# Kernel tuning notes

Measured on AMD Instinct MI355X. Metric: run time of the kernel, lower is better.

The kernel has to match this reference:

```python
import jax, jax.numpy as jnp
import numpy as np

B, S, E, D, OUT = 128, 128, 256, 256, 64


def setup_inputs() -> dict:
    key = jax.random.key(0)
    ks = jax.random.split(key, 10)
    w = lambda k, shp, s=0.05: (jax.random.normal(k, shp, dtype=jnp.float32) * s)
    return {
        "input_encoded": jax.random.normal(ks[0], (B, S, E), dtype=jnp.float32),
        "y_history": jax.random.normal(ks[1], (B, S, OUT), dtype=jnp.float32),
        "h0": jax.random.normal(ks[2], (B, D), dtype=jnp.float32) * 0.1,
        "c0": jax.random.normal(ks[3], (B, D), dtype=jnp.float32) * 0.1,
        "attn_W1": w(ks[4], (2 * D + E, E)),
        "attn_b1": jnp.zeros((E,), jnp.float32),
        "attn_w2": w(ks[5], (E,)),
        "attn_b2": jnp.zeros((1,), jnp.float32),
        "lstm_Wih": w(ks[6], (OUT, 4 * D)),
        "lstm_Whh": w(ks[7], (D, 4 * D)),
        "lstm_bih": jnp.zeros((4 * D,), jnp.float32),
        "lstm_bhh": jnp.zeros((4 * D,), jnp.float32),
        "fc_W": w(ks[8], (E + OUT, OUT)),
        "fc_b": jnp.zeros((OUT,), jnp.float32),
        "fc_out_W": w(ks[9], (D + E, OUT * S)),
        "fc_out_b": jnp.zeros((OUT * S,), jnp.float32),
    }


def reference(input_encoded, y_history, h0, c0, attn_W1, attn_b1, attn_w2, attn_b2,
              lstm_Wih, lstm_Whh, lstm_bih, lstm_bhh, fc_W, fc_b, fc_out_W, fc_out_b):
    # Split the attn first-layer weight according to the concat order (h, c, enc).
    Wh, Wc, We = attn_W1[:D], attn_W1[D:2 * D], attn_W1[2 * D:]
    # Encoder projection is time-invariant across decoder steps; hoist it.
    enc_proj = jnp.einsum('bse,ef->bsf', input_encoded, We)  # [B,S,E]

    def step(carry, y_t):
        h, c, _ = carry
        hc = h @ Wh + c @ Wc + attn_b1                       # [B,E]
        pre = jnp.tanh(enc_proj + hc[:, None, :])            # [B,S,E]
        scores = pre @ attn_w2 + attn_b2[0]                  # [B,S]
        alpha = jax.nn.softmax(scores, axis=1)
        context = jnp.einsum('bs,bse->be', alpha, input_encoded)  # [B,E]
        y_tilde = jnp.concatenate([context, y_t], axis=1) @ fc_W + fc_b  # [B,OUT]
        gates = y_tilde @ lstm_Wih + lstm_bih + h @ lstm_Whh + lstm_bhh  # [B,4D]
        i, f, g, o = jnp.split(gates, 4, axis=1)  # pytorch gate order i,f,g,o
        c_new = jax.nn.sigmoid(f) * c + jax.nn.sigmoid(i) * jnp.tanh(g)
        h_new = jax.nn.sigmoid(o) * jnp.tanh(c_new)
        return (h_new, c_new, context), None

    y_seq = jnp.transpose(y_history, (1, 0, 2))  # [S,B,OUT]
    (h_T, c_T, context_T), _ = jax.lax.scan(step, (h0, c0, jnp.zeros((B, E), h0.dtype)), y_seq)
    out = jnp.concatenate([h_T, context_T], axis=1) @ fc_out_W + fc_out_b  # [B,OUT*S]
    return out.reshape(-1, S, OUT)
```

## Files before the change

kernel.cpp:

```cpp
#include <hip/hip_runtime.h>

#define BB 128
#define SS 128
#define EE 256
#define DD 256
#define OO 64

#define W1_OFF   0
#define WHH_OFF  196608
#define WIH_OFF  458752
#define FCW_OFF  524288
#define WTOTAL   544768

__device__ __forceinline__ float fsig(float x) { return 1.0f / (1.0f + __expf(-x)); }
__device__ __forceinline__ float ftanh(float x) {
    float t = __expf(-2.0f * fabsf(x));
    float r = (1.0f - t) / (1.0f + t);
    return copysignf(r, x);
}
__device__ __forceinline__ int SWZ(int e) { return (e & ~31) | ((e + 4 * (e >> 5)) & 31); }
__device__ __forceinline__ float bflo(unsigned int u) { return __uint_as_float(u << 16); }
__device__ __forceinline__ float bfhi(unsigned int u) { return __uint_as_float(u & 0xffff0000u); }

__global__ __launch_bounds__(256) void conv_kernel(
    const float* __restrict__ W1, const float* __restrict__ Whh,
    const float* __restrict__ Wih, const float* __restrict__ fcW,
    unsigned short* __restrict__ out)
{
    const int idx = blockIdx.x * 256 + threadIdx.x;
    float f;
    if      (idx < WHH_OFF)  f = W1[idx];
    else if (idx < WIH_OFF)  f = Whh[idx - WHH_OFF];
    else if (idx < FCW_OFF)  f = Wih[idx - WIH_OFF];
    else if (idx < WTOTAL)   f = fcW[idx - FCW_OFF];
    else return;
    unsigned int u = __float_as_uint(f);
    u = (u + 0x7fffu + ((u >> 16) & 1u)) >> 16;
    out[idx] = (unsigned short)u;
}

__global__ __launch_bounds__(1024, 4) void scan_kernel(
    const float* __restrict__ inp,
    const float* __restrict__ yhist,
    const float* __restrict__ h0, const float* __restrict__ c0,
    const float* __restrict__ W1f,
    const float* __restrict__ b1, const float* __restrict__ w2, const float* __restrict__ b2,
    const float* __restrict__ bih, const float* __restrict__ bhh,
    const float* __restrict__ fcb,
    const unsigned short* __restrict__ wbf,
    float* __restrict__ hctxT)
{
    __shared__ float sh_inp[SS * 260];
    __shared__ float red[5 * 1024];
    __shared__ float sh_h[DD], sh_c[DD];
    __shared__ float sh_hc[EE];
    __shared__ float sh_w2[EE];
    __shared__ float sh_raw[SS];
    __shared__ float sh_ctx[EE];
    __shared__ float sh_y[OO], sh_yt[OO];
    __shared__ float sh_misc[1];

    const int b = blockIdx.x, t = threadIdx.x;
    const float* inp_b = inp + (size_t)b * SS * EE;
    const unsigned short* W1bf  = wbf + W1_OFF;
    const unsigned short* Whhbf = wbf + WHH_OFF;
    const unsigned short* Wihbf = wbf + WIH_OFF;
    const unsigned short* fcWbf = wbf + FCW_OFF;
    const float b2v = b2[0];

    const int c0_1 = (t & 63) * 4,  kg1 = t >> 6;
    const int c0_2 = (t & 255) * 4, kg2 = t >> 8;
    const int s_own = t >> 3, a2 = t & 7, e0 = a2 * 32;
    const int c0_3 = (t & 127) * 2, sg3 = t >> 7;
    const int o4 = (t & 15) * 4, kc3 = t >> 4;

    const float bs_reg  = bih[t] + bhh[t];
    const float fcb_reg = (t < 64) ? fcb[t] : 0.f;

    #pragma unroll
    for (int i = 0; i < 8; ++i) {
        const int idx = i * 1024 + t;
        const int s = idx >> 6, c4 = (idx & 63) * 4;
        *(float4*)&sh_inp[s * 260 + c4] = *(const float4*)(inp_b + (size_t)idx * 4);
    }
    if (t < 256) {
        sh_h[t] = h0[b * 256 + t]; sh_c[t] = c0[b * 256 + t];
        sh_w2[SWZ(t)] = w2[t];
    }
    __syncthreads();

    float er[32];
    #pragma unroll
    for (int j = 0; j < 32; ++j) er[j] = 0.f;
    {
        const float* We = W1f + 512 * 256;
        for (int kc = 0; kc < 16; ++kc) {
            {
                const int row = t >> 6, c4 = (t & 63) * 4;
                *(float4*)&red[row * 256 + c4] =
                    *(const float4*)(We + (size_t)(kc * 16 + row) * 256 + c4);
            }
            __syncthreads();
            for (int k = 0; k < 16; ++k) {
                const float xv = sh_inp[s_own * 260 + kc * 16 + k];
                #pragma unroll
                for (int j4 = 0; j4 < 8; ++j4) {
                    float4 w = *(const float4*)&red[k * 256 + e0 + j4 * 4];
                    er[j4*4+0] += xv * w.x; er[j4*4+1] += xv * w.y;
                    er[j4*4+2] += xv * w.z; er[j4*4+3] += xv * w.w;
                }
            }
            __syncthreads();
        }
        if (t < 256) red[t] = b1[t];
        __syncthreads();
        #pragma unroll
        for (int j4 = 0; j4 < 8; ++j4) {
            float4 v = *(const float4*)&red[e0 + j4 * 4];
            er[j4*4+0] += v.x; er[j4*4+1] += v.y; er[j4*4+2] += v.z; er[j4*4+3] += v.w;
        }
        __syncthreads();
    }

    for (int ts = 0; ts < SS; ++ts) {
        if (t < 64) sh_y[t] = yhist[(size_t)b * SS * OO + ts * OO + t];

        {
            float a0 = 0.f, a1 = 0.f, a2v = 0.f, a3 = 0.f;
            #pragma unroll 8
            for (int k = kg1 * 32; k < kg1 * 32 + 32; ++k) {
                const float xv = (k < 256) ? sh_h[k] : sh_c[k - 256];
                uint2 w = *(const uint2*)(W1bf + (size_t)k * 256 + c0_1);
                a0  += xv * bflo(w.x); a1 += xv * bfhi(w.x);
                a2v += xv * bflo(w.y); a3 += xv * bfhi(w.y);
            }
            *(float4*)&red[kg1 * 256 + c0_1] = make_float4(a0, a1, a2v, a3);
        }
        __syncthreads();
        if (t < 256) {
            float v = 0.f;
            #pragma unroll
            for (int kg = 0; kg < 16; ++kg) v += red[kg * 256 + t];
            sh_hc[SWZ(t)] = v;
        }
        __syncthreads();

        {
            float a0 = 0.f, a1 = 0.f, a2v = 0.f, a3 = 0.f;
            #pragma unroll 8
            for (int k = kg2 * 64; k < kg2 * 64 + 64; ++k) {
                const float hv = sh_h[k];
                uint2 w = *(const uint2*)(Whhbf + (size_t)k * 1024 + c0_2);
                a0  += hv * bflo(w.x); a1 += hv * bfhi(w.x);
                a2v += hv * bflo(w.y); a3 += hv * bfhi(w.y);
            }
            *(float4*)&red[kg2 * 1024 + c0_2] = make_float4(a0, a1, a2v, a3);
        }
        {
            float acc = 0.f;
            #pragma unroll
            for (int j4 = 0; j4 < 8; ++j4) {
                const int phys = e0 + ((j4 * 4 + 4 * a2) & 31);
                float4 hc4 = *(const float4*)&sh_hc[phys];
                float4 w24 = *(const float4*)&sh_w2[phys];
                acc += ftanh(er[j4*4+0] + hc4.x) * w24.x;
                acc += ftanh(er[j4*4+1] + hc4.y) * w24.y;
                acc += ftanh(er[j4*4+2] + hc4.z) * w24.z;
                acc += ftanh(er[j4*4+3] + hc4.w) * w24.w;
            }
            acc += __shfl_xor(acc, 1);
            acc += __shfl_xor(acc, 2);
            acc += __shfl_xor(acc, 4);
            if (a2 == 0) sh_raw[s_own] = __expf(acc + b2v);
        }
        __syncthreads();

        float gh_reg;
        {
            float v = bs_reg;
            #pragma unroll
            for (int kg = 0; kg < 4; ++kg) v += red[kg * 1024 + t];
            gh_reg = v;
        }
        if (t < 64) {
            float v = sh_raw[t] + sh_raw[t + 64];
            #pragma unroll
            for (int m = 32; m > 0; m >>= 1) v += __shfl_xor(v, m);
            if (t == 0) sh_misc[0] = 1.0f / v;
        }
        __syncthreads();

        uint2 wpre[16];
        #pragma unroll
        for (int i = 0; i < 16; ++i)
            wpre[i] = *(const uint2*)(Wihbf + (size_t)(kg2 * 16 + i) * 1024 + c0_2);
        {
            float ax = 0.f, ay = 0.f;
            #pragma unroll
            for (int i = 0; i < 16; ++i) {
                const int s = sg3 * 16 + i;
                const float al = sh_raw[s];
                ax += al * sh_inp[s * 260 + c0_3];
                ay += al * sh_inp[s * 260 + c0_3 + 1];
            }
            *(float2*)&red[sg3 * 256 + c0_3] = make_float2(ax, ay);
        }
        __syncthreads();
        if (t < 256) {
            float v = 0.f;
            #pragma unroll
            for (int sg = 0; sg < 8; ++sg) v += red[sg * 256 + t];
            v *= sh_misc[0];
            sh_ctx[t] = v;
            if (ts == SS - 1) hctxT[(size_t)(256 + t) * 128 + b] = v;
        }
        __syncthreads();

        {
            float a0 = 0.f, a1 = 0.f, a2v = 0.f, a3 = 0.f;
            for (int kk = kc3 * 5; kk < kc3 * 5 + 5; ++kk) {
                const float val = (kk < 256) ? sh_ctx[kk] : sh_y[kk - 256];
                uint2 w = *(const uint2*)(fcWbf + kk * 64 + o4);
                a0  += val * bflo(w.x); a1 += val * bfhi(w.x);
                a2v += val * bflo(w.y); a3 += val * bfhi(w.y);
            }
            *(float4*)&red[kc3 * 64 + o4] = make_float4(a0, a1, a2v, a3);
        }
        __syncthreads();
        if (t < 64) {
            float v = fcb_reg;
            #pragma unroll 16
            for (int kg = 0; kg < 64; ++kg) v += red[kg * 64 + t];
            sh_yt[t] = v;
        }
        __syncthreads();

        {
            float a0 = 0.f, a1 = 0.f, a2v = 0.f, a3 = 0.f;
            #pragma unroll
            for (int i = 0; i < 16; ++i) {
                const float yv = sh_yt[kg2 * 16 + i];
                const uint2 w = wpre[i];
                a0  += yv * bflo(w.x); a1 += yv * bfhi(w.x);
                a2v += yv * bflo(w.y); a3 += yv * bfhi(w.y);
            }
            *(float4*)&red[kg2 * 1024 + c0_2] = make_float4(a0, a1, a2v, a3);
        }
        __syncthreads();
        {
            float g = gh_reg;
            #pragma unroll
            for (int kg = 0; kg < 4; ++kg) g += red[kg * 1024 + t];
            red[4096 + t] = g;
        }
        __syncthreads();
        if (t < 256) {
            const float gi = red[4096 + t], gf = red[4096 + 256 + t];
            const float gg = red[4096 + 512 + t], go = red[4096 + 768 + t];
            const float cn = fsig(gf) * sh_c[t] + fsig(gi) * ftanh(gg);
            sh_c[t] = cn;
            const float hn = fsig(go) * ftanh(cn);
            sh_h[t] = hn;
            if (ts == SS - 1) hctxT[(size_t)t * 128 + b] = hn;
        }
        __syncthreads();
    }
}

__global__ __launch_bounds__(256) void out_gemm(
    const float* __restrict__ AT, const float* __restrict__ W,
    const float* __restrict__ bias, float* __restrict__ out)
{
    __shared__ float Ab[64 * 132];
    __shared__ float Bb[64 * 32];
    const int t = threadIdx.x;
    const int nt = blockIdx.x * 32;
    const int n4 = (t & 7) * 4;
    const int m4 = (t >> 3) * 4;
    float acc[4][4];
    #pragma unroll
    for (int i = 0; i < 4; ++i)
        #pragma unroll
        for (int jj = 0; jj < 4; ++jj) acc[i][jj] = 0.f;

    for (int kc = 0; kc < 8; ++kc) {
        #pragma unroll
        for (int i = 0; i < 8; ++i) {
            const int flat4 = i * 256 + t;
            const int row = flat4 >> 5, mm4 = (flat4 & 31) * 4;
            float4 v = *(const float4*)(AT + (size_t)(kc * 64 + row) * 128 + mm4);
            *(float4*)&Ab[row * 132 + mm4] = v;
        }
        #pragma unroll
        for (int i = 0; i < 2; ++i) {
            const int fl = t + i * 256;
            const int k = fl >> 3, nn4 = (fl & 7) * 4;
            *(float4*)&Bb[k * 32 + nn4] =
                *(const float4*)(W + (size_t)(kc * 64 + k) * 8192 + nt + nn4);
        }
        __syncthreads();
        for (int k = 0; k < 64; ++k) {
            const float4 bv = *(const float4*)&Bb[k * 32 + n4];
            const float4 av = *(const float4*)&Ab[k * 132 + m4];
            acc[0][0] += av.x * bv.x; acc[0][1] += av.x * bv.y; acc[0][2] += av.x * bv.z; acc[0][3] += av.x * bv.w;
            acc[1][0] += av.y * bv.x; acc[1][1] += av.y * bv.y; acc[1][2] += av.y * bv.z; acc[1][3] += av.y * bv.w;
            acc[2][0] += av.z * bv.x; acc[2][1] += av.z * bv.y; acc[2][2] += av.z * bv.z; acc[2][3] += av.z * bv.w;
            acc[3][0] += av.w * bv.x; acc[3][1] += av.w * bv.y; acc[3][2] += av.w * bv.z; acc[3][3] += av.w * bv.w;
        }
        __syncthreads();
    }
    const float4 bb = *(const float4*)(bias + nt + n4);
    #pragma unroll
    for (int i = 0; i < 4; ++i) {
        float4 r;
        r.x = acc[i][0] + bb.x; r.y = acc[i][1] + bb.y;
        r.z = acc[i][2] + bb.z; r.w = acc[i][3] + bb.w;
        *(float4*)(out + (size_t)(m4 + i) * 8192 + nt + n4) = r;
    }
}

extern "C" void kernel_launch(void* const* d_in, const int* in_sizes, int n_in,
                              void* d_out, int out_size, void* d_ws, size_t ws_size,
                              hipStream_t stream) {
    const float* inp = (const float*)d_in[0];
    const float* yh  = (const float*)d_in[1];
    const float* h0  = (const float*)d_in[2];
    const float* c0  = (const float*)d_in[3];
    const float* W1  = (const float*)d_in[4];
    const float* b1  = (const float*)d_in[5];
    const float* w2  = (const float*)d_in[6];
    const float* b2  = (const float*)d_in[7];
    const float* Wih = (const float*)d_in[8];
    const float* Whh = (const float*)d_in[9];
    const float* bih = (const float*)d_in[10];
    const float* bhh = (const float*)d_in[11];
    const float* fcW = (const float*)d_in[12];
    const float* fcb = (const float*)d_in[13];
    const float* foW = (const float*)d_in[14];
    const float* fob = (const float*)d_in[15];

    float* hctxT = (float*)d_ws;
    unsigned short* wbf = (unsigned short*)d_out;

    conv_kernel<<<dim3((WTOTAL + 255) / 256), dim3(256), 0, stream>>>(W1, Whh, Wih, fcW, wbf);
    scan_kernel<<<dim3(BB), dim3(1024), 0, stream>>>(
        inp, yh, h0, c0, W1, b1, w2, b2, bih, bhh, fcb, wbf, hctxT);
    out_gemm<<<dim3(8192 / 32), dim3(256), 0, stream>>>(hctxT, foW, fob, (float*)d_out);
}
```

Measured before the change: 5.672 ms.

## Restructure per-step matvecs with wider loads, shuffle reductions, register-resident weights

```diff
diff --git a/kernel.cpp b/kernel.cpp
--- a/kernel.cpp
+++ b/kernel.cpp
@@ -21,6 +21,13 @@
 __device__ __forceinline__ int SWZ(int e) { return (e & ~31) | ((e + 4 * (e >> 5)) & 31); }
 __device__ __forceinline__ float bflo(unsigned int u) { return __uint_as_float(u << 16); }
 __device__ __forceinline__ float bfhi(unsigned int u) { return __uint_as_float(u & 0xffff0000u); }
+
+__device__ __forceinline__ void fma8(const uint4 w, const float xv, float* acc) {
+    acc[0] += xv * bflo(w.x); acc[1] += xv * bfhi(w.x);
+    acc[2] += xv * bflo(w.y); acc[3] += xv * bfhi(w.y);
+    acc[4] += xv * bflo(w.z); acc[5] += xv * bfhi(w.z);
+    acc[6] += xv * bflo(w.w); acc[7] += xv * bfhi(w.w);
+}
 
 __global__ __launch_bounds__(256) void conv_kernel(
     const float* __restrict__ W1, const float* __restrict__ Whh,
@@ -51,7 +58,8 @@
     float* __restrict__ hctxT)
 {
     __shared__ float sh_inp[SS * 260];
-    __shared__ float red[5 * 1024];
+    __shared__ float red1[16 * 256];
+    __shared__ float sh_bs[1024];
     __shared__ float sh_h[DD], sh_c[DD];
     __shared__ float sh_hc[EE];
     __shared__ float sh_w2[EE];
@@ -67,15 +75,13 @@
     const unsigned short* Wihbf = wbf + WIH_OFF;
     const unsigned short* fcWbf = wbf + FCW_OFF;
     const float b2v = b2[0];
-
-    const int c0_1 = (t & 63) * 4,  kg1 = t >> 6;
-    const int c0_2 = (t & 255) * 4, kg2 = t >> 8;
+    const int lane = t & 63;
+
+    const int e8 = (t & 31) * 8, kc1 = t >> 5;
+    const int cg2 = t >> 3, kg2 = t & 7;
     const int s_own = t >> 3, a2 = t & 7, e0 = a2 * 32;
-    const int c0_3 = (t & 127) * 2, sg3 = t >> 7;
-    const int o4 = (t & 15) * 4, kc3 = t >> 4;
-
-    const float bs_reg  = bih[t] + bhh[t];
-    const float fcb_reg = (t < 64) ? fcb[t] : 0.f;
+    const int e4 = (t & 63) * 4, sg3 = t >> 6;
+    const int kf = (t & 63) * 5, cf = (t >> 6) * 4;
 
     #pragma unroll
     for (int i = 0; i < 8; ++i) {
@@ -87,6 +93,16 @@
         sh_h[t] = h0[b * 256 + t]; sh_c[t] = c0[b * 256 + t];
         sh_w2[SWZ(t)] = w2[t];
     }
+    sh_bs[t] = bih[t] + bhh[t];
+
+    uint4 wih_r[8];
+    #pragma unroll
+    for (int i = 0; i < 8; ++i)
+        wih_r[i] = *(const uint4*)(Wihbf + (size_t)(kg2 * 8 + i) * 1024 + cg2 * 8);
+    uint2 fcw_r[5];
+    #pragma unroll
+    for (int i = 0; i < 5; ++i)
+        fcw_r[i] = *(const uint2*)(fcWbf + (kf + i) * 64 + cf);
     __syncthreads();
 
     float er[32];
@@ -97,7 +113,7 @@
         for (int kc = 0; kc < 16; ++kc) {
             {
                 const int row = t >> 6, c4 = (t & 63) * 4;
-                *(float4*)&red[row * 256 + c4] =
+                *(float4*)&red1[row * 256 + c4] =
                     *(const float4*)(We + (size_t)(kc * 16 + row) * 256 + c4);
             }
             __syncthreads();
@@ -105,18 +121,18 @@
                 const float xv = sh_inp[s_own * 260 + kc * 16 + k];
                 #pragma unroll
                 for (int j4 = 0; j4 < 8; ++j4) {
-                    float4 w = *(const float4*)&red[k * 256 + e0 + j4 * 4];
+                    float4 w = *(const float4*)&red1[k * 256 + e0 + j4 * 4];
                     er[j4*4+0] += xv * w.x; er[j4*4+1] += xv * w.y;
                     er[j4*4+2] += xv * w.z; er[j4*4+3] += xv * w.w;
                 }
             }
             __syncthreads();
         }
-        if (t < 256) red[t] = b1[t];
+        if (t < 256) red1[t] = b1[t];
         __syncthreads();
         #pragma unroll
         for (int j4 = 0; j4 < 8; ++j4) {
-            float4 v = *(const float4*)&red[e0 + j4 * 4];
+            float4 v = *(const float4*)&red1[e0 + j4 * 4];
             er[j4*4+0] += v.x; er[j4*4+1] += v.y; er[j4*4+2] += v.z; er[j4*4+3] += v.w;
         }
         __syncthreads();
@@ -126,61 +142,70 @@
         if (t < 64) sh_y[t] = yhist[(size_t)b * SS * OO + ts * OO + t];
 
         {
-            float a0 = 0.f, a1 = 0.f, a2v = 0.f, a3 = 0.f;
-            #pragma unroll 8
-            for (int k = kg1 * 32; k < kg1 * 32 + 32; ++k) {
+            float acc[8];
+            #pragma unroll
+            for (int r = 0; r < 8; ++r) acc[r] = 0.f;
+            #pragma unroll 4
+            for (int k = kc1 * 16; k < kc1 * 16 + 16; ++k) {
                 const float xv = (k < 256) ? sh_h[k] : sh_c[k - 256];
-                uint2 w = *(const uint2*)(W1bf + (size_t)k * 256 + c0_1);
-                a0  += xv * bflo(w.x); a1 += xv * bfhi(w.x);
-                a2v += xv * bflo(w.y); a3 += xv * bfhi(w.y);
-            }
-            *(float4*)&red[kg1 * 256 + c0_1] = make_float4(a0, a1, a2v, a3);
+                uint4 w = *(const uint4*)(W1bf + (size_t)k * 256 + e8);
+                fma8(w, xv, acc);
+            }
+            #pragma unroll
+            for (int r = 0; r < 8; ++r) acc[r] += __shfl_xor(acc[r], 32);
+            if ((t & 32) == 0) {
+                *(float4*)&red1[(kc1 >> 1) * 256 + e8]     = make_float4(acc[0], acc[1], acc[2], acc[3]);
+                *(float4*)&red1[(kc1 >> 1) * 256 + e8 + 4] = make_float4(acc[4], acc[5], acc[6], acc[7]);
+            }
         }
         __syncthreads();
         if (t < 256) {
             float v = 0.f;
             #pragma unroll
-            for (int kg = 0; kg < 16; ++kg) v += red[kg * 256 + t];
+            for (int r = 0; r < 16; ++r) v += red1[r * 256 + t];
             sh_hc[SWZ(t)] = v;
         }
         __syncthreads();
 
+        float g[8];
+        #pragma unroll
+        for (int r = 0; r < 8; ++r) g[r] = 0.f;
+        #pragma unroll 8
+        for (int i = 0; i < 32; ++i) {
+            const int k = kg2 * 32 + ((i + 4 * kg2) & 31);
+            const float hv = sh_h[k];
+            uint4 w = *(const uint4*)(Whhbf + (size_t)k * 1024 + cg2 * 8);
+            fma8(w, hv, g);
+        }
         {
-            float a0 = 0.f, a1 = 0.f, a2v = 0.f, a3 = 0.f;
-            #pragma unroll 8
-            for (int k = kg2 * 64; k < kg2 * 64 + 64; ++k) {
-                const float hv = sh_h[k];
-                uint2 w = *(const uint2*)(Whhbf + (size_t)k * 1024 + c0_2);
-                a0  += hv * bflo(w.x); a1 += hv * bfhi(w.x);
-                a2v += hv * bflo(w.y); a3 += hv * bfhi(w.y);
-            }
-            *(float4*)&red[kg2 * 1024 + c0_2] = make_float4(a0, a1, a2v, a3);
-        }
-        {
-            float acc = 0.f;
+            float sacc = 0.f;
             #pragma unroll
             for (int j4 = 0; j4 < 8; ++j4) {
                 const int phys = e0 + ((j4 * 4 + 4 * a2) & 31);
                 float4 hc4 = *(const float4*)&sh_hc[phys];
                 float4 w24 = *(const float4*)&sh_w2[phys];
-                acc += ftanh(er[j4*4+0] + hc4.x) * w24.x;
-                acc += ftanh(er[j4*4+1] + hc4.y) * w24.y;
-                acc += ftanh(er[j4*4+2] + hc4.z) * w24.z;
-                acc += ftanh(er[j4*4+3] + hc4.w) * w24.w;
-            }
-            acc += __shfl_xor(acc, 1);
-            acc += __shfl_xor(acc, 2);
-            acc += __shfl_xor(acc, 4);
-            if (a2 == 0) sh_raw[s_own] = __expf(acc + b2v);
-        }
-        __syncthreads();
-
-        float gh_reg;
+                sacc += ftanh(er[j4*4+0] + hc4.x) * w24.x;
+                sacc += ftanh(er[j4*4+1] + hc4.y) * w24.y;
+                sacc += ftanh(er[j4*4+2] + hc4.z) * w24.z;
+                sacc += ftanh(er[j4*4+3] + hc4.w) * w24.w;
+            }
+            sacc += __shfl_xor(sacc, 1);
+            sacc += __shfl_xor(sacc, 2);
+            sacc += __shfl_xor(sacc, 4);
+            if (a2 == 0) sh_raw[s_own] = __expf(sacc + b2v);
+        }
+        __syncthreads();
+
         {
-            float v = bs_reg;
-            #pragma unroll
-            for (int kg = 0; kg < 4; ++kg) v += red[kg * 1024 + t];
-            gh_reg = v;
+            float ax = 0.f, ay = 0.f, az = 0.f, aw = 0.f;
+            #pragma unroll
+            for (int i = 0; i < 8; ++i) {
+                const int s = sg3 * 8 + i;
+                const float al = sh_raw[s];
+                float4 iv = *(const float4*)&sh_inp[s * 260 + e4];
+                ax += al * iv.x; ay += al * iv.y; az += al * iv.z; aw += al * iv.w;
+            }
+            *(float4*)&red1[sg3 * 256 + e4] = make_float4(ax, ay, az, aw);
         }
         if (t < 64) {
             float v = sh_raw[t] + sh_raw[t + 64];
@@ -189,27 +214,10 @@
             if (t == 0) sh_misc[0] = 1.0f / v;
         }
         __syncthreads();
-
-        uint2 wpre[16];
-        #pragma unroll
-        for (int i = 0; i < 16; ++i)
-            wpre[i] = *(const uint2*)(Wihbf + (size_t)(kg2 * 16 + i) * 1024 + c0_2);
-        {
-            float ax = 0.f, ay = 0.f;
-            #pragma unroll
-            for (int i = 0; i < 16; ++i) {
-                const int s = sg3 * 16 + i;
-                const float al = sh_raw[s];
-                ax += al * sh_inp[s * 260 + c0_3];
-                ay += al * sh_inp[s * 260 + c0_3 + 1];
-            }
-            *(float2*)&red[sg3 * 256 + c0_3] = make_float2(ax, ay);
-        }
-        __syncthreads();
         if (t < 256) {
             float v = 0.f;
             #pragma unroll
-            for (int sg = 0; sg < 8; ++sg) v += red[sg * 256 + t];
+            for (int r = 0; r < 16; ++r) v += red1[r * 256 + t];
             v *= sh_misc[0];
             sh_ctx[t] = v;
             if (ts == SS - 1) hctxT[(size_t)(256 + t) * 128 + b] = v;
@@ -218,45 +226,48 @@
 
         {
             float a0 = 0.f, a1 = 0.f, a2v = 0.f, a3 = 0.f;
-            for (int kk = kc3 * 5; kk < kc3 * 5 + 5; ++kk) {
-                const float val = (kk < 256) ? sh_ctx[kk] : sh_y[kk - 256];
-                uint2 w = *(const uint2*)(fcWbf + kk * 64 + o4);
+            #pragma unroll
+            for (int i = 0; i < 5; ++i) {
+                const int k = kf + i;
+                const float val = (k < 256) ? sh_ctx[k] : sh_y[k - 256];
+                const uint2 w = fcw_r[i];
                 a0  += val * bflo(w.x); a1 += val * bfhi(w.x);
                 a2v += val * bflo(w.y); a3 += val * bfhi(w.y);
             }
-            *(float4*)&red[kc3 * 64 + o4] = make_float4(a0, a1, a2v, a3);
-        }
-        __syncthreads();
-        if (t < 64) {
-            float v = fcb_reg;
-            #pragma unroll 16
-            for (int kg = 0; kg < 64; ++kg) v += red[kg * 64 + t];
-            sh_yt[t] = v;
-        }
-        __syncthreads();
-
-        {
-            float a0 = 0.f, a1 = 0.f, a2v = 0.f, a3 = 0.f;
-            #pragma unroll
-            for (int i = 0; i < 16; ++i) {
-                const float yv = sh_yt[kg2 * 16 + i];
-                const uint2 w = wpre[i];
-                a0  += yv * bflo(w.x); a1 += yv * bfhi(w.x);
-                a2v += yv * bflo(w.y); a3 += yv * bfhi(w.y);
-            }
-            *(float4*)&red[kg2 * 1024 + c0_2] = make_float4(a0, a1, a2v, a3);
-        }
-        __syncthreads();
-        {
-            float g = gh_reg;
-            #pragma unroll
-            for (int kg = 0; kg < 4; ++kg) g += red[kg * 1024 + t];
-            red[4096 + t] = g;
+            #pragma unroll
+            for (int m = 1; m < 64; m <<= 1) {
+                a0  += __shfl_xor(a0, m);  a1 += __shfl_xor(a1, m);
+                a2v += __shfl_xor(a2v, m); a3 += __shfl_xor(a3, m);
+            }
+            if (lane == 0) {
+                float4 r; r.x = a0 + fcb[cf]; r.y = a1 + fcb[cf + 1];
+                r.z = a2v + fcb[cf + 2]; r.w = a3 + fcb[cf + 3];
+                *(float4*)&sh_yt[cf] = r;
+            }
+        }
+        __syncthreads();
+
+        #pragma unroll
+        for (int i = 0; i < 8; ++i) {
+            const float yv = sh_yt[kg2 * 8 + i];
+            fma8(wih_r[i], yv, g);
+        }
+        #pragma unroll
+        for (int r = 0; r < 8; ++r) {
+            g[r] += __shfl_xor(g[r], 1);
+            g[r] += __shfl_xor(g[r], 2);
+            g[r] += __shfl_xor(g[r], 4);
+        }
+        if (kg2 == 0) {
+            *(float4*)&red1[cg2 * 8]     = make_float4(g[0], g[1], g[2], g[3]);
+            *(float4*)&red1[cg2 * 8 + 4] = make_float4(g[4], g[5], g[6], g[7]);
         }
         __syncthreads();
         if (t < 256) {
-            const float gi = red[4096 + t], gf = red[4096 + 256 + t];
-            const float gg = red[4096 + 512 + t], go = red[4096 + 768 + t];
+            const float gi = red1[t]       + sh_bs[t];
+            const float gf = red1[256 + t] + sh_bs[256 + t];
+            const float gg = red1[512 + t] + sh_bs[512 + t];
+            const float go = red1[768 + t] + sh_bs[768 + t];
             const float cn = fsig(gf) * sh_c[t] + fsig(gi) * ftanh(gg);
             sh_c[t] = cn;
             const float hn = fsig(go) * ftanh(cn);
```

Result: faster. 5.483 ms (-3.3%).

## Keep bf16 recurrent weights resident in registers and reduce partial sums with shuffles

Applied to the files above, without the earlier changes.

```diff
diff --git a/kernel.cpp b/kernel.cpp
--- a/kernel.cpp
+++ b/kernel.cpp
@@ -12,6 +12,8 @@
 #define FCW_OFF  524288
 #define WTOTAL   544768
 
+#define PIN4(v_) asm volatile("" : "+v"((v_).x), "+v"((v_).y), "+v"((v_).z), "+v"((v_).w))
+
 __device__ __forceinline__ float fsig(float x) { return 1.0f / (1.0f + __expf(-x)); }
 __device__ __forceinline__ float ftanh(float x) {
     float t = __expf(-2.0f * fabsf(x));
@@ -21,6 +23,13 @@
 __device__ __forceinline__ int SWZ(int e) { return (e & ~31) | ((e + 4 * (e >> 5)) & 31); }
 __device__ __forceinline__ float bflo(unsigned int u) { return __uint_as_float(u << 16); }
 __device__ __forceinline__ float bfhi(unsigned int u) { return __uint_as_float(u & 0xffff0000u); }
+
+__device__ __forceinline__ void fma8(const uint4 w, const float xv, float* acc) {
+    acc[0] += xv * bflo(w.x); acc[1] += xv * bfhi(w.x);
+    acc[2] += xv * bflo(w.y); acc[3] += xv * bfhi(w.y);
+    acc[4] += xv * bflo(w.z); acc[5] += xv * bfhi(w.z);
+    acc[6] += xv * bflo(w.w); acc[7] += xv * bfhi(w.w);
+}
 
 __global__ __launch_bounds__(256) void conv_kernel(
     const float* __restrict__ W1, const float* __restrict__ Whh,
@@ -50,13 +59,13 @@
     const unsigned short* __restrict__ wbf,
     float* __restrict__ hctxT)
 {
-    __shared__ float sh_inp[SS * 260];
-    __shared__ float red[5 * 1024];
+    __shared__ float sh_inp[SS * EE];
+    __shared__ float red[16 * 256];
     __shared__ float sh_h[DD], sh_c[DD];
     __shared__ float sh_hc[EE];
     __shared__ float sh_w2[EE];
+    __shared__ float sh_ctx[EE];
     __shared__ float sh_raw[SS];
-    __shared__ float sh_ctx[EE];
     __shared__ float sh_y[OO], sh_yt[OO];
     __shared__ float sh_misc[1];
 
@@ -68,25 +77,55 @@
     const unsigned short* fcWbf = wbf + FCW_OFF;
     const float b2v = b2[0];
 
-    const int c0_1 = (t & 63) * 4,  kg1 = t >> 6;
-    const int c0_2 = (t & 255) * 4, kg2 = t >> 8;
+    const int wv = t >> 6, lane = t & 63;
+
+    const int kg1 = lane >> 1, c1b = wv * 16 + (lane & 1) * 8;
+    const int kgb = lane >> 3, cbb = wv * 64 + (lane & 7) * 8;
     const int s_own = t >> 3, a2 = t & 7, e0 = a2 * 32;
-    const int c0_3 = (t & 127) * 2, sg3 = t >> 7;
+    const int e4 = (t & 63) * 4, sc = t >> 6;
     const int o4 = (t & 15) * 4, kc3 = t >> 4;
 
-    const float bs_reg  = bih[t] + bhh[t];
-    const float fcb_reg = (t < 64) ? fcb[t] : 0.f;
+    uint4 w1r[16];
+    #pragma unroll
+    for (int i = 0; i < 16; ++i)
+        w1r[i] = *(const uint4*)(W1bf + (size_t)(kg1 * 16 + i) * 256 + c1b);
+    uint4 whr[32];
+    #pragma unroll
+    for (int i = 0; i < 32; ++i)
+        whr[i] = *(const uint4*)(Whhbf + (size_t)(kgb * 32 + i) * 1024 + cbb);
+    uint4 wir[8];
+    #pragma unroll
+    for (int i = 0; i < 8; ++i)
+        wir[i] = *(const uint4*)(Wihbf + (size_t)(kgb * 8 + i) * 1024 + cbb);
+    uint2 fwr[5];
+    #pragma unroll
+    for (int i = 0; i < 5; ++i)
+        fwr[i] = *(const uint2*)(fcWbf + (kc3 * 5 + i) * 64 + o4);
+    #pragma unroll
+    for (int i = 0; i < 16; ++i) PIN4(w1r[i]);
+    #pragma unroll
+    for (int i = 0; i < 32; ++i) PIN4(whr[i]);
+    #pragma unroll
+    for (int i = 0; i < 8; ++i)  PIN4(wir[i]);
+    #pragma unroll
+    for (int i = 0; i < 5; ++i)  asm volatile("" : "+v"(fwr[i].x), "+v"(fwr[i].y));
 
     #pragma unroll
     for (int i = 0; i < 8; ++i) {
         const int idx = i * 1024 + t;
         const int s = idx >> 6, c4 = (idx & 63) * 4;
-        *(float4*)&sh_inp[s * 260 + c4] = *(const float4*)(inp_b + (size_t)idx * 4);
+        *(float4*)&sh_inp[s * 256 + c4] = *(const float4*)(inp_b + (size_t)idx * 4);
     }
     if (t < 256) {
         sh_h[t] = h0[b * 256 + t]; sh_c[t] = c0[b * 256 + t];
         sh_w2[SWZ(t)] = w2[t];
     }
+    float bs4[4] = {0.f, 0.f, 0.f, 0.f};
+    if (t < 256) {
+        #pragma unroll
+        for (int q = 0; q < 4; ++q) bs4[q] = bih[q * 256 + t] + bhh[q * 256 + t];
+    }
+    const float fcb_reg = (t < 64) ? fcb[t] : 0.f;
     __syncthreads();
 
     float er[32];
@@ -102,7 +141,7 @@
             }
             __syncthreads();
             for (int k = 0; k < 16; ++k) {
-                const float xv = sh_inp[s_own * 260 + kc * 16 + k];
+                const float xv = sh_inp[s_own * 256 + kc * 16 + k];
                 #pragma unroll
                 for (int j4 = 0; j4 < 8; ++j4) {
                     float4 w = *(const float4*)&red[k * 256 + e0 + j4 * 4];
@@ -126,36 +165,32 @@
         if (t < 64) sh_y[t] = yhist[(size_t)b * SS * OO + ts * OO + t];
 
         {
-            float a0 = 0.f, a1 = 0.f, a2v = 0.f, a3 = 0.f;
-            #pragma unroll 8
-            for (int k = kg1 * 32; k < kg1 * 32 + 32; ++k) {
-                const float xv = (k < 256) ? sh_h[k] : sh_c[k - 256];
-                uint2 w = *(const uint2*)(W1bf + (size_t)k * 256 + c0_1);
-                a0  += xv * bflo(w.x); a1 += xv * bfhi(w.x);
-                a2v += xv * bflo(w.y); a3 += xv * bfhi(w.y);
-            }
-            *(float4*)&red[kg1 * 256 + c0_1] = make_float4(a0, a1, a2v, a3);
-        }
-        __syncthreads();
-        if (t < 256) {
-            float v = 0.f;
-            #pragma unroll
-            for (int kg = 0; kg < 16; ++kg) v += red[kg * 256 + t];
-            sh_hc[SWZ(t)] = v;
-        }
-        __syncthreads();
-
-        {
-            float a0 = 0.f, a1 = 0.f, a2v = 0.f, a3 = 0.f;
-            #pragma unroll 8
-            for (int k = kg2 * 64; k < kg2 * 64 + 64; ++k) {
-                const float hv = sh_h[k];
-                uint2 w = *(const uint2*)(Whhbf + (size_t)k * 1024 + c0_2);
-                a0  += hv * bflo(w.x); a1 += hv * bfhi(w.x);
-                a2v += hv * bflo(w.y); a3 += hv * bfhi(w.y);
-            }
-            *(float4*)&red[kg2 * 1024 + c0_2] = make_float4(a0, a1, a2v, a3);
-        }
+            float acc[8];
+            #pragma unroll
+            for (int r = 0; r < 8; ++r) acc[r] = 0.f;
+            const float* xsrc = (kg1 < 16) ? &sh_h[kg1 * 16] : &sh_c[kg1 * 16 - 256];
+            #pragma unroll
+            for (int i = 0; i < 16; ++i) fma8(w1r[i], xsrc[i], acc);
+            #pragma unroll
+            for (int m = 2; m <= 32; m <<= 1) {
+                #pragma unroll
+                for (int r = 0; r < 8; ++r) acc[r] += __shfl_xor(acc[r], m);
+            }
+            if (lane < 2) {
+                *(float4*)&sh_hc[SWZ(c1b)]     = make_float4(acc[0], acc[1], acc[2], acc[3]);
+                *(float4*)&sh_hc[SWZ(c1b + 4)] = make_float4(acc[4], acc[5], acc[6], acc[7]);
+            }
+        }
+        float g[8];
+        #pragma unroll
+        for (int r = 0; r < 8; ++r) g[r] = 0.f;
+        {
+            const float* hsrc = &sh_h[kgb * 32];
+            #pragma unroll
+            for (int i = 0; i < 32; ++i) fma8(whr[i], hsrc[i], g);
+        }
+        __syncthreads();
+
         {
             float acc = 0.f;
             #pragma unroll
@@ -174,14 +209,6 @@
             if (a2 == 0) sh_raw[s_own] = __expf(acc + b2v);
         }
         __syncthreads();
-
-        float gh_reg;
-        {
-            float v = bs_reg;
-            #pragma unroll
-            for (int kg = 0; kg < 4; ++kg) v += red[kg * 1024 + t];
-            gh_reg = v;
-        }
         if (t < 64) {
             float v = sh_raw[t] + sh_raw[t + 64];
             #pragma unroll
@@ -190,26 +217,22 @@
         }
         __syncthreads();
 
-        uint2 wpre[16];
-        #pragma unroll
-        for (int i = 0; i < 16; ++i)
-            wpre[i] = *(const uint2*)(Wihbf + (size_t)(kg2 * 16 + i) * 1024 + c0_2);
-        {
-            float ax = 0.f, ay = 0.f;
-            #pragma unroll
-            for (int i = 0; i < 16; ++i) {
-                const int s = sg3 * 16 + i;
+        {
+            float ax = 0.f, ay = 0.f, az = 0.f, aw = 0.f;
+            #pragma unroll
+            for (int i = 0; i < 8; ++i) {
+                const int s = sc * 8 + i;
                 const float al = sh_raw[s];
-                ax += al * sh_inp[s * 260 + c0_3];
-                ay += al * sh_inp[s * 260 + c0_3 + 1];
-            }
-            *(float2*)&red[sg3 * 256 + c0_3] = make_float2(ax, ay);
+                float4 iv = *(const float4*)&sh_inp[s * 256 + e4];
+                ax += al * iv.x; ay += al * iv.y; az += al * iv.z; aw += al * iv.w;
+            }
+            *(float4*)&red[sc * 256 + e4] = make_float4(ax, ay, az, aw);
         }
         __syncthreads();
         if (t < 256) {
             float v = 0.f;
             #pragma unroll
-            for (int sg = 0; sg < 8; ++sg) v += red[sg * 256 + t];
+            for (int k = 0; k < 16; ++k) v += red[k * 256 + t];
             v *= sh_misc[0];
             sh_ctx[t] = v;
             if (ts == SS - 1) hctxT[(size_t)(256 + t) * 128 + b] = v;
@@ -217,46 +240,46 @@
         __syncthreads();
 
         {
-            float a0 = 0.f, a1 = 0.f, a2v = 0.f, a3 = 0.f;
-            for (int kk = kc3 * 5; kk < kc3 * 5 + 5; ++kk) {
+            float acc[4] = {0.f, 0.f, 0.f, 0.f};
+            #pragma unroll
+            for (int i = 0; i < 5; ++i) {
+                const int kk = kc3 * 5 + i;
                 const float val = (kk < 256) ? sh_ctx[kk] : sh_y[kk - 256];
-                uint2 w = *(const uint2*)(fcWbf + kk * 64 + o4);
-                a0  += val * bflo(w.x); a1 += val * bfhi(w.x);
-                a2v += val * bflo(w.y); a3 += val * bfhi(w.y);
-            }
-            *(float4*)&red[kc3 * 64 + o4] = make_float4(a0, a1, a2v, a3);
+                const uint2 w = fwr[i];
+                acc[0] += val * bflo(w.x); acc[1] += val * bfhi(w.x);
+                acc[2] += val * bflo(w.y); acc[3] += val * bfhi(w.y);
+            }
+            *(float4*)&red[kc3 * 64 + o4] = make_float4(acc[0], acc[1], acc[2], acc[3]);
         }
         __syncthreads();
         if (t < 64) {
             float v = fcb_reg;
             #pragma unroll 16
-            for (int kg = 0; kg < 64; ++kg) v += red[kg * 64 + t];
+            for (int kc = 0; kc < 64; ++kc) v += red[kc * 64 + t];
             sh_yt[t] = v;
         }
         __syncthreads();
 
         {
-            float a0 = 0.f, a1 = 0.f, a2v = 0.f, a3 = 0.f;
-            #pragma unroll
-            for (int i = 0; i < 16; ++i) {
-                const float yv = sh_yt[kg2 * 16 + i];
-                const uint2 w = wpre[i];
-                a0  += yv * bflo(w.x); a1 += yv * bfhi(w.x);
-                a2v += yv * bflo(w.y); a3 += yv * bfhi(w.y);
-            }
-            *(float4*)&red[kg2 * 1024 + c0_2] = make_float4(a0, a1, a2v, a3);
-        }
-        __syncthreads();
-        {
-            float g = gh_reg;
-            #pragma unroll
-            for (int kg = 0; kg < 4; ++kg) g += red[kg * 1024 + t];
-            red[4096 + t] = g;
+            const float* ysrc = &sh_yt[kgb * 8];
+            #pragma unroll
+            for (int i = 0; i < 8; ++i) fma8(wir[i], ysrc[i], g);
+            #pragma unroll
+            for (int m = 8; m <= 32; m <<= 1) {
+                #pragma unroll
+                for (int r = 0; r < 8; ++r) g[r] += __shfl_xor(g[r], m);
+            }
+            if (lane < 8) {
+                *(float4*)&red[wv * 64 + lane * 8]     = make_float4(g[0], g[1], g[2], g[3]);
+                *(float4*)&red[wv * 64 + lane * 8 + 4] = make_float4(g[4], g[5], g[6], g[7]);
+            }
         }
         __syncthreads();
         if (t < 256) {
-            const float gi = red[4096 + t], gf = red[4096 + 256 + t];
-            const float gg = red[4096 + 512 + t], go = red[4096 + 768 + t];
+            const float gi = red[t]       + bs4[0];
+            const float gf = red[256 + t] + bs4[1];
+            const float gg = red[512 + t] + bs4[2];
+            const float go = red[768 + t] + bs4[3];
             const float cn = fsig(gf) * sh_c[t] + fsig(gi) * ftanh(gg);
             sh_c[t] = cn;
             const float hn = fsig(go) * ftanh(cn);
```

After: 16.32 ms. 2.88x slower.
